# Kernel tuning notes

Measured on AMD Instinct MI355X. Metric: run time of the kernel, lower is better.

The kernel has to match this reference:

```python
import jax, jax.numpy as jnp
import numpy as np

TAU = 100.0
DT = 1.0
NOISE_STD = 0.1
HID = 100


def setup_inputs() -> dict:
    key = jax.random.key(0)
    ks = jax.random.split(key, 7)
    T, B = 750, 1024
    input_seq = jax.random.normal(ks[0], (T, B, 4), dtype=jnp.float32)
    noise = jax.random.normal(ks[1], (T, B, HID), dtype=jnp.float32)
    # orthogonal recurrent weight J [H, H]
    a = jax.random.normal(ks[2], (HID, HID), dtype=jnp.float32)
    q, r = jnp.linalg.qr(a)
    J_w = q * jnp.sign(jnp.diag(r))[None, :]
    # input projection rows [b_m; b_c; b_cm; b_cc] -> [4, H] (xavier for (H,1) fan)
    bound_b = float(np.sqrt(6.0 / (HID + 1)))
    Bmat = jax.random.uniform(ks[3], (4, HID), jnp.float32, -bound_b, bound_b)
    c_x = jnp.zeros((HID,), dtype=jnp.float32)
    bound_w = float(np.sqrt(6.0 / (HID + 1)))
    Wout_w = jax.random.uniform(ks[4], (1, HID), jnp.float32, -bound_w, bound_w)
    Wout_b = jnp.zeros((1,), dtype=jnp.float32)
    return {"input_seq": input_seq, "noise": noise, "J_w": J_w,
            "Bmat": Bmat, "c_x": c_x, "Wout_w": Wout_w, "Wout_b": Wout_b}


def reference(input_seq, noise, J_w, Bmat, c_x, Wout_w, Wout_b):
    # input_seq: [T, B, 4], noise: [T, B, H]
    T, B, _ = input_seq.shape
    alpha = DT / TAU

    # precompute input drive for all steps: u_m@b_m^T + ... == u_t @ Bmat  [T, B, H]
    drive = jnp.einsum('tbi,ih->tbh', input_seq, Bmat)

    def step(x, inp):
        d_t, n_t = inp
        r = jnp.tanh(x)
        dx = alpha * (-x + r @ J_w.T + d_t + c_x + NOISE_STD * n_t)
        x = x + dx
        return x, None

    x0 = jnp.zeros((B, HID), dtype=input_seq.dtype)
    x_final, _ = jax.lax.scan(step, x0, (drive, noise))
    out = jnp.tanh(x_final) @ Wout_w.T + Wout_b  # [B, 1]
    return out.squeeze(-1)  # [B]
```

## Files before the change

kernel.cpp:

```cpp
#include <hip/hip_runtime.h>
#include <hip/hip_bf16.h>

#define HID 100
#define TT 750
#define NBT 1024
#define ALPHA 0.01f
#define NSTD 0.1f

typedef __bf16 bf16x8 __attribute__((ext_vector_type(8)));
typedef float floatx4 __attribute__((ext_vector_type(4)));

__device__ __forceinline__ float fast_tanh(float v) {
    float e = __expf(2.0f * v);
    return 1.0f - 2.0f / (e + 1.0f);
}

#define MFMA(A, B, C) __builtin_amdgcn_mfma_f32_16x16x32_bf16((A), (B), (C), 0, 0, 0)

__global__ __launch_bounds__(448)
void rnn_kernel(const float* __restrict__ useq,
                const float* __restrict__ noise,
                const float* __restrict__ Jw,
                const float* __restrict__ Bm,
                const float* __restrict__ cxp,
                const float* __restrict__ Ww,
                const float* __restrict__ Wb,
                float* __restrict__ out)
{
    __shared__ __align__(16) __bf16 abuf[2][16][128];
    __shared__ float red[4][112];

    const int tid  = threadIdx.x;
    const int wv   = tid >> 6;
    const int lane = tid & 63;
    const int m16  = lane & 15;
    const int q    = lane >> 4;
    const int h    = wv * 16 + m16;
    const bool act = (h < HID);
    const int gb0  = blockIdx.x * 4;

    for (int i = tid; i < 512; i += 448)
        ((floatx4*)abuf)[i] = floatx4{0.f, 0.f, 0.f, 0.f};

    bf16x8 jhi[4], jlo[4];
    #pragma unroll
    for (int s = 0; s < 4; ++s) {
        bf16x8 vh = {}; bf16x8 vl = {};
        #pragma unroll
        for (int j = 0; j < 8; ++j) {
            const int k = s * 32 + q * 8 + j;
            float a = (act && k < HID) ? Jw[h * HID + k] : 0.0f;
            const __bf16 hi = (__bf16)a;
            vh[j] = hi;
            vl[j] = (__bf16)(a - (float)hi);
        }
        jhi[s] = vh; jlo[s] = vl;
    }

    float bm0=0.f, bm1=0.f, bm2=0.f, bm3=0.f, cx=0.f;
    if (act) {
        bm0 = Bm[0*HID + h]; bm1 = Bm[1*HID + h];
        bm2 = Bm[2*HID + h]; bm3 = Bm[3*HID + h];
        cx  = cxp[h];
    }

    const float* nptr = noise + (size_t)(gb0 + q) * HID + (act ? h : (HID - 1));
    const floatx4* uptr = (const floatx4*)(useq + (size_t)(gb0 + q) * 4);
    float n0=0.f, n1=0.f, n2=0.f, n3=0.f;
    if (act) {
        n0 = nptr[(size_t)0 * NBT * HID];
        n1 = nptr[(size_t)1 * NBT * HID];
        n2 = nptr[(size_t)2 * NBT * HID];
        n3 = nptr[(size_t)3 * NBT * HID];
    }
    floatx4 u0 = uptr[(size_t)0 * NBT];
    floatx4 u1 = uptr[(size_t)1 * NBT];

    int rdo[4];
    #pragma unroll
    for (int s = 0; s < 4; ++s)
        rdo[s] = m16 * 128 + (((4 * s + q) ^ (m16 & 7)) << 3);
    const int wro = (4 * q) * 128 + ((((h >> 3) ^ ((4 * q) & 7)) << 3) | (h & 7));

    float x = 0.f;
    const floatx4 kz = {0.f, 0.f, 0.f, 0.f};
    __syncthreads();

    auto body = [&](int t, int p, float& nr, floatx4& ur) {
        const float d = cx + ur[0]*bm0 + ur[1]*bm1 + ur[2]*bm2 + ur[3]*bm3
                      + NSTD * nr;
        floatx4 c0 = kz; c0[0] = d;

        const __bf16* ab = &abuf[p][0][0];
        bf16x8 afr[4];
        #pragma unroll
        for (int s = 0; s < 4; ++s)
            afr[s] = *(const bf16x8*)(ab + rdo[s]);

        floatx4 ah0 = MFMA(afr[1], jhi[1], MFMA(afr[0], jhi[0], c0));
        floatx4 ah1 = MFMA(afr[3], jhi[3], MFMA(afr[2], jhi[2], kz));
        floatx4 al0 = MFMA(afr[1], jlo[1], MFMA(afr[0], jlo[0], kz));
        floatx4 al1 = MFMA(afr[3], jlo[3], MFMA(afr[2], jlo[2], kz));
        const float y = (ah0[0] + ah1[0]) + (al0[0] + al1[0]);

        if (act) {
            x = x * (1.f - ALPHA) + ALPHA * y;
            const float r = fast_tanh(x);
            abuf[p ^ 1][0][wro] = (__bf16)r;
            const int tn = (t + 4 <= TT - 1) ? (t + 4) : (TT - 1);
            nr = nptr[(size_t)tn * NBT * HID];
        }
        {
            const int tu = (t + 2 <= TT - 1) ? (t + 2) : (TT - 1);
            ur = uptr[(size_t)tu * NBT];
        }
        asm volatile("s_waitcnt lgkmcnt(0)\n\ts_barrier" ::: "memory");
    };

    for (int t4 = 0; t4 < 748; t4 += 4) {
        body(t4 + 0, 0, n0, u0);
        body(t4 + 1, 1, n1, u1);
        body(t4 + 2, 0, n2, u0);
        body(t4 + 3, 1, n3, u1);
    }
    body(748, 0, n0, u0);
    body(749, 1, n1, u1);

    if (act) red[q][h] = fast_tanh(x) * Ww[h];
    __syncthreads();
    if (tid < 4) {
        float s = Wb[0];
        #pragma unroll 4
        for (int i = 0; i < HID; ++i) s += red[tid][i];
        out[gb0 + tid] = s;
    }
}

extern "C" void kernel_launch(void* const* d_in, const int* in_sizes, int n_in,
                              void* d_out, int out_size, void* d_ws, size_t ws_size,
                              hipStream_t stream) {
    rnn_kernel<<<dim3(256), dim3(448), 0, stream>>>(
        (const float*)d_in[0], (const float*)d_in[1], (const float*)d_in[2],
        (const float*)d_in[3], (const float*)d_in[4], (const float*)d_in[5],
        (const float*)d_in[6], (float*)d_out);
}
```

Before: 827.7 us.

## Halve batch per block to two rows and double grid to 512 blocks

```diff
diff --git a/kernel.cpp b/kernel.cpp
--- a/kernel.cpp
+++ b/kernel.cpp
@@ -27,8 +27,8 @@
                 const float* __restrict__ Wb,
                 float* __restrict__ out)
 {
-    __shared__ __align__(16) __bf16 abuf[2][16][128];
-    __shared__ float red[4][112];
+    __shared__ __align__(16) __bf16 abuf[2][2][128];
+    __shared__ float red[2][112];
 
     const int tid  = threadIdx.x;
     const int wv   = tid >> 6;
@@ -36,11 +36,10 @@
     const int m16  = lane & 15;
     const int q    = lane >> 4;
     const int h    = wv * 16 + m16;
-    const bool act = (h < HID);
-    const int gb0  = blockIdx.x * 4;
+    const bool act = (q < 2) && (h < HID);
+    const int gb0  = blockIdx.x * 2;
 
-    for (int i = tid; i < 512; i += 448)
-        ((floatx4*)abuf)[i] = floatx4{0.f, 0.f, 0.f, 0.f};
+    if (tid < 64) ((floatx4*)abuf)[tid] = floatx4{0.f, 0.f, 0.f, 0.f};
 
     bf16x8 jhi[4], jlo[4];
     #pragma unroll
@@ -49,7 +48,7 @@
         #pragma unroll
         for (int j = 0; j < 8; ++j) {
             const int k = s * 32 + q * 8 + j;
-            float a = (act && k < HID) ? Jw[h * HID + k] : 0.0f;
+            float a = (h < HID && k < HID) ? Jw[h * HID + k] : 0.0f;
             const __bf16 hi = (__bf16)a;
             vh[j] = hi;
             vl[j] = (__bf16)(a - (float)hi);
@@ -64,53 +63,49 @@
         cx  = cxp[h];
     }
 
-    const float* nptr = noise + (size_t)(gb0 + q) * HID + (act ? h : (HID - 1));
-    const floatx4* uptr = (const floatx4*)(useq + (size_t)(gb0 + q) * 4);
+    const float* nptr = noise + (size_t)(gb0 + (q & 1)) * HID + (act ? h : 0);
+    const floatx4* uptr = (const floatx4*)(useq + (size_t)(gb0 + (q & 1)) * 4);
     float n0=0.f, n1=0.f, n2=0.f, n3=0.f;
+    floatx4 u0 = {0,0,0,0}, u1 = {0,0,0,0};
     if (act) {
         n0 = nptr[(size_t)0 * NBT * HID];
         n1 = nptr[(size_t)1 * NBT * HID];
         n2 = nptr[(size_t)2 * NBT * HID];
         n3 = nptr[(size_t)3 * NBT * HID];
+        u0 = uptr[(size_t)0 * NBT];
+        u1 = uptr[(size_t)1 * NBT];
     }
-    floatx4 u0 = uptr[(size_t)0 * NBT];
-    floatx4 u1 = uptr[(size_t)1 * NBT];
-
-    int rdo[4];
-    #pragma unroll
-    for (int s = 0; s < 4; ++s)
-        rdo[s] = m16 * 128 + (((4 * s + q) ^ (m16 & 7)) << 3);
-    const int wro = (4 * q) * 128 + ((((h >> 3) ^ ((4 * q) & 7)) << 3) | (h & 7));
 
     float x = 0.f;
-    const floatx4 kz = {0.f, 0.f, 0.f, 0.f};
     __syncthreads();
 
     auto body = [&](int t, int p, float& nr, floatx4& ur) {
-        const float d = cx + ur[0]*bm0 + ur[1]*bm1 + ur[2]*bm2 + ur[3]*bm3
-                      + NSTD * nr;
-        floatx4 c0 = kz; c0[0] = d;
-
-        const __bf16* ab = &abuf[p][0][0];
-        bf16x8 afr[4];
-        #pragma unroll
-        for (int s = 0; s < 4; ++s)
-            afr[s] = *(const bf16x8*)(ab + rdo[s]);
-
-        floatx4 ah0 = MFMA(afr[1], jhi[1], MFMA(afr[0], jhi[0], c0));
-        floatx4 ah1 = MFMA(afr[3], jhi[3], MFMA(afr[2], jhi[2], kz));
-        floatx4 al0 = MFMA(afr[1], jlo[1], MFMA(afr[0], jlo[0], kz));
-        floatx4 al1 = MFMA(afr[3], jlo[3], MFMA(afr[2], jlo[2], kz));
-        const float y = (ah0[0] + ah1[0]) + (al0[0] + al1[0]);
+        bf16x8 afr[4] = {{}, {}, {}, {}};
+        if (m16 < 2) {
+            const __bf16* ab = &abuf[p][0][0];
+            #pragma unroll
+            for (int s = 0; s < 4; ++s)
+                afr[s] = *(const bf16x8*)(ab + m16 * 128 + (4 * s + q) * 8);
+        }
+        const floatx4 z = {0.f, 0.f, 0.f, 0.f};
+        floatx4 ah0 = MFMA(afr[1], jhi[1], MFMA(afr[0], jhi[0], z));
+        floatx4 ah1 = MFMA(afr[3], jhi[3], MFMA(afr[2], jhi[2], z));
+        floatx4 al0 = MFMA(afr[1], jlo[1], MFMA(afr[0], jlo[0], z));
+        floatx4 al1 = MFMA(afr[3], jlo[3], MFMA(afr[2], jlo[2], z));
+        const float y0 = (ah0[0] + ah1[0]) + (al0[0] + al1[0]);
+        const float y1 = (ah0[1] + ah1[1]) + (al0[1] + al1[1]);
+        const float y1s = __int_as_float(
+            __builtin_amdgcn_ds_swizzle(__float_as_int(y1), 0x401F));
+        const float y = (q == 0) ? y0 : y1s;
 
         if (act) {
-            x = x * (1.f - ALPHA) + ALPHA * y;
+            const float d = cx + ur[0]*bm0 + ur[1]*bm1 + ur[2]*bm2 + ur[3]*bm3
+                          + NSTD * nr;
+            x = x * (1.f - ALPHA) + ALPHA * (y + d);
             const float r = fast_tanh(x);
-            abuf[p ^ 1][0][wro] = (__bf16)r;
+            abuf[p ^ 1][q][h] = (__bf16)r;
             const int tn = (t + 4 <= TT - 1) ? (t + 4) : (TT - 1);
             nr = nptr[(size_t)tn * NBT * HID];
-        }
-        {
             const int tu = (t + 2 <= TT - 1) ? (t + 2) : (TT - 1);
             ur = uptr[(size_t)tu * NBT];
         }
@@ -128,7 +123,7 @@
 
     if (act) red[q][h] = fast_tanh(x) * Ww[h];
     __syncthreads();
-    if (tid < 4) {
+    if (tid < 2) {
         float s = Wb[0];
         #pragma unroll 4
         for (int i = 0; i < HID; ++i) s += red[tid][i];
@@ -139,7 +134,7 @@
 extern "C" void kernel_launch(void* const* d_in, const int* in_sizes, int n_in,
                               void* d_out, int out_size, void* d_ws, size_t ws_size,
                               hipStream_t stream) {
-    rnn_kernel<<<dim3(256), dim3(448), 0, stream>>>(
+    rnn_kernel<<<dim3(512), dim3(448), 0, stream>>>(
         (const float*)d_in[0], (const float*)d_in[1], (const float*)d_in[2],
         (const float*)d_in[3], (const float*)d_in[4], (const float*)d_in[5],
         (const float*)d_in[6], (float*)d_out);
```

Result: faster. 765.3 us (-7.5%).
